# Optimization experiments

Hardware: AMD Instinct MI355X
Metric: run time of the kernel (lower is better)

## Reference

```python
import jax, jax.numpy as jnp
import numpy as np

NUM_HEADS = 8

def _spline_scores(x):
    # x: (BH, S, E), softmax-normalized. Kernel per pair (i,j):
    #   sum_{e,f} [ max*min + 0.5*min^2*max - min^3/6 ] + E^2
    # using min*max = a*b  =>  a*b*(1 + 0.5*min) - min^3/6
    E = x.shape[-1]
    xi = x[:, :, None, :, None]          # (BH, S, 1, E, 1)
    xj = x[:, None, :, None, :]          # (BH, 1, S, 1, E)
    m = jnp.minimum(xi, xj)              # (BH, S, S, E, E)
    k = xi * xj * (1.0 + 0.5 * m) - (m * m * m) * (1.0 / 6.0)
    return k.sum(axis=(-1, -2)) + jnp.asarray(E * E, x.dtype)  # (BH, S, S)

def setup_inputs() -> dict:
    key = jax.random.key(0)
    k1, k2, k3 = jax.random.split(key, 3)
    B, S, D = 2, 128, 256
    scale = 1.0 / np.sqrt(D)
    return {
        "inputs": jax.random.normal(k1, (B, S, D), dtype=jnp.float32),
        "w_in": jax.random.normal(k2, (D, D), dtype=jnp.float32) * scale,
        "b_in": jnp.zeros((D,), dtype=jnp.float32),
        "w_out": jax.random.normal(k3, (D, D), dtype=jnp.float32) * scale,
        "b_out": jnp.zeros((D,), dtype=jnp.float32),
    }

def reference(inputs, w_in, b_in, w_out, b_out):
    B, S, D = inputs.shape
    H = NUM_HEADS
    E = D // H
    x = jnp.einsum('bsd,ed->bse', inputs, w_in) + b_in          # in_project (torch Linear: x @ W.T + b)
    x = x.reshape(B, S, H, E).transpose(0, 2, 1, 3).reshape(B * H, S, E)
    x = jax.nn.softmax(x, axis=-1)
    attn = _spline_scores(x) / E                                 # (BH, S, S)
    attn = jax.nn.softmax(attn, axis=-1)                         # dropout is identity at inference
    out = jnp.einsum('bij,bje->bie', attn, x)                    # (BH, S, E)
    out = out.reshape(B, H, S, E).transpose(0, 2, 1, 3).reshape(B, S, D)
    return jnp.einsum('bsd,ed->bse', out, w_out) + b_out
```

## Files before the change

kernel.cpp:

```cpp
#include <hip/hip_runtime.h>
#include <math.h>

constexpr int BB = 2;
constexpr int SS = 128;
constexpr int DD = 256;
constexpr int HH = 8;
constexpr int EE = 32;
constexpr int PKG = 132;

__global__ __launch_bounds__(256) void spline_ka(
    const float* __restrict__ inp,
    const float* __restrict__ w_in,
    const float* __restrict__ b_in,
    float* __restrict__ xs_out,
    float* __restrict__ pkg_g)
{
  const int row = blockIdx.x;
  const int e = threadIdx.x;
  __shared__ float in_row[DD];
  __shared__ float vals[DD];
  __shared__ float exps[DD];

  in_row[e] = inp[row * DD + e];
  __syncthreads();

  const float* wr = w_in + e * DD;
  float acc = b_in[e];
#pragma unroll 8
  for (int d = 0; d < DD; d += 4) {
    const float4 w4 = *reinterpret_cast<const float4*>(wr + d);
    acc = fmaf(in_row[d + 0], w4.x, acc);
    acc = fmaf(in_row[d + 1], w4.y, acc);
    acc = fmaf(in_row[d + 2], w4.z, acc);
    acc = fmaf(in_row[d + 3], w4.w, acc);
  }
  vals[e] = acc;
  __syncthreads();

  const int h = e >> 5, base = h * EE, l = e & 31;
  float mx = -1e30f;
#pragma unroll
  for (int k = 0; k < EE; ++k) mx = fmaxf(mx, vals[base + k]);
  const float ex = __expf(acc - mx);
  exps[e] = ex;
  __syncthreads();
  float sum = 0.f;
#pragma unroll
  for (int k = 0; k < EE; ++k) sum += exps[base + k];
  const float x = ex / sum;

  const int b = row >> 7, s = row & 127;
  const int bh = b * HH + h;
  xs_out[(bh * SS + s) * EE + l] = x;

  float v = x;
#pragma unroll
  for (int k = 2; k <= 32; k <<= 1) {
#pragma unroll
    for (int j = k >> 1; j > 0; j >>= 1) {
      const float o = __shfl_xor(v, j, 32);
      const bool up = ((l & k) == 0);
      const bool tmin = (((l & j) == 0) == up);
      v = tmin ? fminf(v, o) : fmaxf(v, o);
    }
  }
  float i1 = v, i2 = v * v, i3 = v * v * v;
#pragma unroll
  for (int j = 1; j < 32; j <<= 1) {
    const float o1 = __shfl_up(i1, j, 32);
    const float o2 = __shfl_up(i2, j, 32);
    const float o3 = __shfl_up(i3, j, 32);
    if (l >= j) { i1 += o1; i2 += o2; i3 += o3; }
  }
  float* pk = pkg_g + (bh * SS + s) * PKG;
  pk[l] = v;
  pk[32 + l + 1] = i1;
  pk[65 + l + 1] = i2;
  pk[98 + l + 1] = i3;
  if (l == 0) { pk[32] = 0.f; pk[65] = 0.f; pk[98] = 0.f; }
}

__global__ __launch_bounds__(128) void spline_kb(
    const float* __restrict__ xs_g,
    const float* __restrict__ pkg_g,
    float* __restrict__ y)
{
  const int i = blockIdx.x;
  const int bh = blockIdx.y;
  const int t = threadIdx.x;

  __shared__ float xs[SS * EE];
  __shared__ float pkv[131];
  __shared__ float at[SS];
  __shared__ float part[128];
  __shared__ float wred[4];

  const float4* s4 = (const float4*)(xs_g + bh * SS * EE);
  float4* x4 = (float4*)xs;
#pragma unroll
  for (int k = 0; k < 8; ++k) x4[t + 128 * k] = s4[t + 128 * k];
  const float* pk = pkg_g + (bh * SS + i) * PKG;
  if (t < 131) pkv[t] = pk[t];
  float vreg[EE];
  {
    const float4* vr4 = (const float4*)(xs_g + (bh * SS + t) * EE);
    float4* vv = (float4*)vreg;
#pragma unroll
    for (int k = 0; k < 8; ++k) vv[k] = vr4[k];
  }
  __syncthreads();

  const float* sI = pkv;
  const float* P1 = pkv + 32;
  const float* P2 = pkv + 65;
  const float* P3 = pkv + 98;
  const float T1 = P1[32];

  float A = 0.f, B = 0.f, C = 0.f, Dg = 0.f, sv = 0.f;
#pragma unroll
  for (int bb = 0; bb < EE; ++bb) {
    const float v = vreg[bb];
    sv += v;
    int idx = 0;
#pragma unroll
    for (int off = 16; off > 0; off >>= 1)
      if (sI[idx + off - 1] <= v) idx += off;
    if (sI[idx] <= v) ++idx;
    const float g1 = P1[idx], g2 = P2[idx], g3 = P3[idx];
    const float v2 = v * v;
    const float fi = (float)idx - 32.0f;
    A = fmaf(v, g2, A);
    B = fmaf(v2, T1 - g1, B);
    C = fmaf(v2 * v, fi, C);
    Dg += g3;
  }
  const float sumF = fmaf(0.5f, A + B, (C - Dg) * (1.f / 6.f));
  const float logit = (fmaf(T1, sv, sumF) + (float)(EE * EE)) * (1.0f / (float)EE);

  float mx = logit;
#pragma unroll
  for (int off = 32; off; off >>= 1) mx = fmaxf(mx, __shfl_xor(mx, off));
  const int wid = t >> 6;
  if ((t & 63) == 0) wred[wid] = mx;
  __syncthreads();
  mx = fmaxf(wred[0], wred[1]);

  const float ex = __expf(logit - mx);
  float sm = ex;
#pragma unroll
  for (int off = 32; off; off >>= 1) sm += __shfl_xor(sm, off);
  __syncthreads();
  if ((t & 63) == 0) wred[2 + wid] = sm;
  at[t] = ex;
  __syncthreads();
  const float rs = 1.0f / (wred[2] + wred[3]);

  const int e = t & 31, q = t >> 5;
  float o = 0.f;
#pragma unroll
  for (int jj = 0; jj < 32; ++jj) {
    const int j = q * 32 + jj;
    o = fmaf(at[j], xs[j * EE + e], o);
  }
  part[t] = o;
  __syncthreads();
  if (t < EE) {
    const float oo = (part[t] + part[t + 32] + part[t + 64] + part[t + 96]) * rs;
    const int b = bh >> 3, h = bh & 7;
    y[(b * SS + i) * DD + h * EE + t] = oo;
  }
}

__global__ __launch_bounds__(256) void spline_k3(
    const float* __restrict__ y,
    const float* __restrict__ w_out,
    const float* __restrict__ b_out,
    float* __restrict__ out)
{
  const int row = blockIdx.x;
  const int e = threadIdx.x;
  __shared__ float yr[DD];
  yr[e] = y[row * DD + e];
  __syncthreads();

  const float* wr = w_out + e * DD;
  float acc = b_out[e];
#pragma unroll 8
  for (int d = 0; d < DD; d += 4) {
    const float4 w4 = *reinterpret_cast<const float4*>(wr + d);
    acc = fmaf(yr[d + 0], w4.x, acc);
    acc = fmaf(yr[d + 1], w4.y, acc);
    acc = fmaf(yr[d + 2], w4.z, acc);
    acc = fmaf(yr[d + 3], w4.w, acc);
  }
  out[row * DD + e] = acc;
}

extern "C" void kernel_launch(void* const* d_in, const int* in_sizes, int n_in,
                              void* d_out, int out_size, void* d_ws, size_t ws_size,
                              hipStream_t stream) {
  const float* inp   = (const float*)d_in[0];
  const float* w_in  = (const float*)d_in[1];
  const float* b_in  = (const float*)d_in[2];
  const float* w_out = (const float*)d_in[3];
  const float* b_out = (const float*)d_in[4];
  float* out = (float*)d_out;

  float* ws_x   = (float*)d_ws;
  float* ws_pkg = ws_x + BB * HH * SS * EE;
  float* ws_y   = ws_pkg + BB * HH * SS * PKG;

  spline_ka<<<BB * SS, 256, 0, stream>>>(inp, w_in, b_in, ws_x, ws_pkg);
  spline_kb<<<dim3(SS, BB * HH), 128, 0, stream>>>(ws_x, ws_pkg, ws_y);
  spline_k3<<<BB * SS, 256, 0, stream>>>(ws_y, w_out, b_out, out);
}
```

Measured before the change: 91.88 us.

## Fuse attention-score kernel with output projection into one per-row block

Merges the per-(i,bh) score/softmax/AV kernel and the output projection kernel into a single kernel in which each block handles one query row across all eight heads with 1024 threads. The head outputs are assembled in shared memory and multiplied by w_out directly, split into four K segments. This removes one launch and the round trip of the intermediate y buffer through global memory. The xs tile is no longer staged in shared memory; the AV product now reads xs from global memory. The grid shrinks to 256 large blocks, which may reduce occupancy and parallelism.

```diff
diff --git a/kernel.cpp b/kernel.cpp
--- a/kernel.cpp
+++ b/kernel.cpp
@@ -80,43 +80,47 @@
   if (l == 0) { pk[32] = 0.f; pk[65] = 0.f; pk[98] = 0.f; }
 }
 
-__global__ __launch_bounds__(128) void spline_kb(
+__global__ __launch_bounds__(1024) void spline_kb3(
     const float* __restrict__ xs_g,
     const float* __restrict__ pkg_g,
-    float* __restrict__ y)
+    const float* __restrict__ w_out,
+    const float* __restrict__ b_out,
+    float* __restrict__ out)
 {
   const int i = blockIdx.x;
-  const int bh = blockIdx.y;
-  const int t = threadIdx.x;
-
-  __shared__ float xs[SS * EE];
-  __shared__ float pkv[131];
-  __shared__ float at[SS];
-  __shared__ float part[128];
-  __shared__ float wred[4];
-
-  const float4* s4 = (const float4*)(xs_g + bh * SS * EE);
-  float4* x4 = (float4*)xs;
-#pragma unroll
-  for (int k = 0; k < 8; ++k) x4[t + 128 * k] = s4[t + 128 * k];
-  const float* pk = pkg_g + (bh * SS + i) * PKG;
-  if (t < 131) pkv[t] = pk[t];
+  const int b = blockIdx.y;
+  const int tid = threadIdx.x;
+  const int h = tid >> 7;
+  const int j = tid & 127;
+  const int bh = b * HH + h;
+
+  __shared__ float pkv[HH * PKG];
+  __shared__ float at[HH * SS];
+  __shared__ float part[1024];
+  __shared__ float yrow[DD];
+  __shared__ float wredm[16];
+  __shared__ float wreds[16];
+
+  for (int idx = tid; idx < HH * 131; idx += 1024) {
+    const int hh = idx / 131, kk = idx - hh * 131;
+    pkv[hh * PKG + kk] = pkg_g[((b * HH + hh) * SS + i) * PKG + kk];
+  }
   float vreg[EE];
   {
-    const float4* vr4 = (const float4*)(xs_g + (bh * SS + t) * EE);
+    const float4* vr4 = (const float4*)(xs_g + (bh * SS + j) * EE);
     float4* vv = (float4*)vreg;
 #pragma unroll
     for (int k = 0; k < 8; ++k) vv[k] = vr4[k];
   }
   __syncthreads();
 
-  const float* sI = pkv;
-  const float* P1 = pkv + 32;
-  const float* P2 = pkv + 65;
-  const float* P3 = pkv + 98;
+  const float* sI = pkv + h * PKG;
+  const float* P1 = sI + 32;
+  const float* P2 = sI + 65;
+  const float* P3 = sI + 98;
   const float T1 = P1[32];
 
-  float A = 0.f, B = 0.f, C = 0.f, Dg = 0.f, sv = 0.f;
+  float A = 0.f, Bq = 0.f, C = 0.f, Dg = 0.f, sv = 0.f;
 #pragma unroll
   for (int bb = 0; bb < EE; ++bb) {
     const float v = vreg[bb];
@@ -130,70 +134,66 @@
     const float v2 = v * v;
     const float fi = (float)idx - 32.0f;
     A = fmaf(v, g2, A);
-    B = fmaf(v2, T1 - g1, B);
+    Bq = fmaf(v2, T1 - g1, Bq);
     C = fmaf(v2 * v, fi, C);
     Dg += g3;
   }
-  const float sumF = fmaf(0.5f, A + B, (C - Dg) * (1.f / 6.f));
+  const float sumF = fmaf(0.5f, A + Bq, (C - Dg) * (1.f / 6.f));
   const float logit = (fmaf(T1, sv, sumF) + (float)(EE * EE)) * (1.0f / (float)EE);
 
   float mx = logit;
 #pragma unroll
   for (int off = 32; off; off >>= 1) mx = fmaxf(mx, __shfl_xor(mx, off));
-  const int wid = t >> 6;
-  if ((t & 63) == 0) wred[wid] = mx;
-  __syncthreads();
-  mx = fmaxf(wred[0], wred[1]);
-
+  if ((tid & 63) == 0) wredm[tid >> 6] = mx;
+  __syncthreads();
+  mx = fmaxf(wredm[h * 2], wredm[h * 2 + 1]);
   const float ex = __expf(logit - mx);
+  at[tid] = ex;
   float sm = ex;
 #pragma unroll
   for (int off = 32; off; off >>= 1) sm += __shfl_xor(sm, off);
-  __syncthreads();
-  if ((t & 63) == 0) wred[2 + wid] = sm;
-  at[t] = ex;
-  __syncthreads();
-  const float rs = 1.0f / (wred[2] + wred[3]);
-
-  const int e = t & 31, q = t >> 5;
-  float o = 0.f;
-#pragma unroll
-  for (int jj = 0; jj < 32; ++jj) {
-    const int j = q * 32 + jj;
-    o = fmaf(at[j], xs[j * EE + e], o);
-  }
-  part[t] = o;
-  __syncthreads();
-  if (t < EE) {
-    const float oo = (part[t] + part[t + 32] + part[t + 64] + part[t + 96]) * rs;
-    const int b = bh >> 3, h = bh & 7;
-    y[(b * SS + i) * DD + h * EE + t] = oo;
-  }
-}
-
-__global__ __launch_bounds__(256) void spline_k3(
-    const float* __restrict__ y,
-    const float* __restrict__ w_out,
-    const float* __restrict__ b_out,
-    float* __restrict__ out)
-{
-  const int row = blockIdx.x;
-  const int e = threadIdx.x;
-  __shared__ float yr[DD];
-  yr[e] = y[row * DD + e];
-  __syncthreads();
-
-  const float* wr = w_out + e * DD;
-  float acc = b_out[e];
-#pragma unroll 8
-  for (int d = 0; d < DD; d += 4) {
-    const float4 w4 = *reinterpret_cast<const float4*>(wr + d);
-    acc = fmaf(yr[d + 0], w4.x, acc);
-    acc = fmaf(yr[d + 1], w4.y, acc);
-    acc = fmaf(yr[d + 2], w4.z, acc);
-    acc = fmaf(yr[d + 3], w4.w, acc);
-  }
-  out[row * DD + e] = acc;
+  if ((tid & 63) == 0) wreds[tid >> 6] = sm;
+  __syncthreads();
+
+  {
+    const int e = tid & 31, q = (tid >> 5) & 3;
+    const float* xb = xs_g + (bh * SS + q * 32) * EE + e;
+    const float* ab = at + h * SS + q * 32;
+    float o = 0.f;
+#pragma unroll
+    for (int jj = 0; jj < 32; ++jj)
+      o = fmaf(ab[jj], xb[jj * EE], o);
+    part[tid] = o;
+  }
+  __syncthreads();
+  if (tid < DD) {
+    const int hh = tid >> 5, ee = tid & 31;
+    const float rs = 1.0f / (wreds[hh * 2] + wreds[hh * 2 + 1]);
+    const float* pp = part + hh * SS + ee;
+    yrow[tid] = (pp[0] + pp[32] + pp[64] + pp[96]) * rs;
+  }
+  __syncthreads();
+
+  {
+    const int f = tid & 255, seg = tid >> 8;
+    const float* wr = w_out + f * DD + seg * 64;
+    const float* yb = yrow + seg * 64;
+    float accp = 0.f;
+#pragma unroll
+    for (int k = 0; k < 64; k += 4) {
+      const float4 w4 = *reinterpret_cast<const float4*>(wr + k);
+      accp = fmaf(yb[k + 0], w4.x, accp);
+      accp = fmaf(yb[k + 1], w4.y, accp);
+      accp = fmaf(yb[k + 2], w4.z, accp);
+      accp = fmaf(yb[k + 3], w4.w, accp);
+    }
+    part[tid] = accp;
+  }
+  __syncthreads();
+  if (tid < DD) {
+    out[(b * SS + i) * DD + tid] =
+        b_out[tid] + part[tid] + part[256 + tid] + part[512 + tid] + part[768 + tid];
+  }
 }
 
 extern "C" void kernel_launch(void* const* d_in, const int* in_sizes, int n_in,
@@ -208,9 +208,7 @@
 
   float* ws_x   = (float*)d_ws;
   float* ws_pkg = ws_x + BB * HH * SS * EE;
-  float* ws_y   = ws_pkg + BB * HH * SS * PKG;
 
   spline_ka<<<BB * SS, 256, 0, stream>>>(inp, w_in, b_in, ws_x, ws_pkg);
-  spline_kb<<<dim3(SS, BB * HH), 128, 0, stream>>>(ws_x, ws_pkg, ws_y);
-  spline_k3<<<BB * SS, 256, 0, stream>>>(ws_y, w_out, b_out, out);
+  spline_kb3<<<dim3(SS, BB), 1024, 0, stream>>>(ws_x, ws_pkg, w_out, b_out, out);
 }
```

After: 93.30 us. Within noise of the previous version (+1.5%).
